# Optimization experiments

Measured on AMD Instinct MI355X. Metric: run time of the kernel, lower is better.

The kernel has to match this reference:

```python
import jax, jax.numpy as jnp
import numpy as np

N, E, F, H, C, G = 50000, 800000, 128, 64, 10, 512
NEG_SLOPE = 0.2
BN_EPS = 1e-5


def setup_inputs() -> dict:
    key = jax.random.key(0)
    ks = jax.random.split(key, 20)
    s = 0.05
    inp = {
        "x": jax.random.normal(ks[0], (N, F), jnp.float32),
        "edge_index": jax.random.randint(ks[1], (2, E), 0, N),
        "batch": jnp.sort(jax.random.randint(ks[2], (N,), 0, G)),
        # GATv2 layer 1 (lin_l, lin_r, att, bias)
        "Wl1": jax.random.normal(ks[3], (H, F), jnp.float32) * s,
        "Wr1": jax.random.normal(ks[4], (H, F), jnp.float32) * s,
        "att1": jax.random.normal(ks[5], (H,), jnp.float32) * s,
        "b1": jnp.zeros((H,), jnp.float32),
        # GATv2 layer 2
        "Wl2": jax.random.normal(ks[6], (H, H), jnp.float32) * s,
        "Wr2": jax.random.normal(ks[7], (H, H), jnp.float32) * s,
        "att2": jax.random.normal(ks[8], (H,), jnp.float32) * s,
        "b2": jnp.zeros((H,), jnp.float32),
        # MLP head: Linear(H,H) -> BatchNorm1d(H) -> ReLU -> Linear(H,C)
        "W3": jax.random.normal(ks[9], (H, H), jnp.float32) * s,
        "b3": jnp.zeros((H,), jnp.float32),
        "gamma": jnp.ones((H,), jnp.float32),
        "beta": jnp.zeros((H,), jnp.float32),
        "W4": jax.random.normal(ks[10], (C, H), jnp.float32) * s,
        "b4": jnp.zeros((C,), jnp.float32),
    }
    return inp


def _gatv2_layer(x, src, dst, Wl, Wr, att, b, n_nodes):
    # GATv2: e_ij = att . LeakyReLU(Wl x_j + Wr x_i); softmax over j in N(i); out_i = sum alpha_ij * Wl x_j
    xl = x @ Wl.T  # [N, H] source transform
    xr = x @ Wr.T  # [N, H] dest transform
    e = jnp.einsum("eh,h->e", jax.nn.leaky_relu(xl[src] + xr[dst], NEG_SLOPE), att)  # [E]
    m = jax.ops.segment_max(e, dst, num_segments=n_nodes)
    m = jnp.where(jnp.isfinite(m), m, 0.0)
    a = jnp.exp(e - m[dst])
    denom = jax.ops.segment_sum(a, dst, num_segments=n_nodes)
    alpha = a / denom[dst]  # self-loops guarantee denom > 0
    out = jax.ops.segment_sum(alpha[:, None] * xl[src], dst, num_segments=n_nodes)
    return out + b


def reference(x, edge_index, batch, Wl1, Wr1, att1, b1, Wl2, Wr2, att2, b2,
              W3, b3, gamma, beta, W4, b4):
    n_nodes = x.shape[0]
    loop = jnp.arange(n_nodes, dtype=edge_index.dtype)
    src = jnp.concatenate([edge_index[0], loop])  # add_self_loops=True (PyG default)
    dst = jnp.concatenate([edge_index[1], loop])

    h = _gatv2_layer(x, src, dst, Wl1, Wr1, att1, b1, n_nodes)
    h = jax.nn.relu(h)
    h = _gatv2_layer(h, src, dst, Wl2, Wr2, att2, b2, n_nodes)

    # global_mean_pool over graphs
    sums = jax.ops.segment_sum(h, batch, num_segments=G)  # [G, H]
    counts = jax.ops.segment_sum(jnp.ones((n_nodes,), h.dtype), batch, num_segments=G)
    pooled = sums / jnp.maximum(counts, 1.0)[:, None]

    # MLP head: Linear -> BatchNorm1d (training: batch stats, biased var) -> ReLU -> Linear
    z = pooled @ W3.T + b3
    mu = jnp.mean(z, axis=0)
    var = jnp.mean((z - mu) ** 2, axis=0)
    z = (z - mu) / jnp.sqrt(var + BN_EPS) * gamma + beta
    z = jax.nn.relu(z)
    z = z @ W4.T + b4
    return jax.nn.log_softmax(z, axis=1)
```

## Files before the change

kernel.cpp:

```cpp
#include <hip/hip_runtime.h>
#include <hip/hip_bf16.h>

#define NODES 50000
#define EDGES 800000
#define FEAT 128
#define HID 64
#define NCLS 10
#define NGRAPH 512
#define ETOT (EDGES + NODES)
#define NEG_SLOPE 0.2f
#define BN_EPS 1e-5f
#define NT_TILES ((NODES + 63) / 64)
#define NBINS 98
#define BTILE 8192
#define BBLK ((ETOT + BTILE - 1) / BTILE)
#define BIN_CAP 14336
#define TBLK 512
#define EDGE_WAVES 8192

typedef __attribute__((ext_vector_type(8))) short short8;
typedef __attribute__((ext_vector_type(4))) float f32x4;

__device__ __forceinline__ short f2b(float v) {
  unsigned int u = __float_as_uint(v);
  return (short)((u + 0x7FFFu + ((u >> 16) & 1u)) >> 16);
}
__device__ __forceinline__ float b2f(short s) {
  return __uint_as_float(((unsigned int)(unsigned short)s) << 16);
}


__device__ __forceinline__ void transform_body(
    char* smem, int bid, const void* __restrict__ A, int a_bf16, int K,
    const float* __restrict__ Wl, const float* __restrict__ Wr,
    short* __restrict__ xl, short* __restrict__ xr) {
  short* s_a = (short*)smem;
  char* dyn2 = smem + 64 * (K + 8) * 2;
  short* s_w = (short*)dyn2;
  float* s_out = (float*)dyn2;
  const int pitch = K + 8;
  int tid = threadIdx.x;
  int w = tid >> 6, lane = tid & 63;
  int n16 = lane & 15, quad = lane >> 4;
  int half = w & 1, chunk = w >> 1;
  short* outp = half ? xr : xl;
  float* s_ow = s_out + w * 16 * 68;
  int ktn = K >> 5;
  int kq = K >> 2, ksh = (K == 128) ? 5 : 4;

  for (int i = tid; i < 128 * kq; i += 512) {
    int r = i / kq, c = i - r * kq;
    const float* src = (r < 64) ? Wl : Wr;
    float4 v = *((const float4*)(src + (r & 63) * K) + c);
    short4 bb;
    bb.x = f2b(v.x); bb.y = f2b(v.y); bb.z = f2b(v.z); bb.w = f2b(v.w);
    *(short4*)(s_w + r * pitch + c * 4) = bb;
  }
  __syncthreads();
  short8 bfrag[4][4];
  for (int t = 0; t < 4; ++t)
    for (int kt = 0; kt < ktn; ++kt)
      bfrag[t][kt] = *(const short8*)(s_w + (half * 64 + t * 16 + n16) * pitch + kt * 32 + quad * 8);

  for (int nt = bid; nt < NT_TILES; nt += TBLK) {
    int n0 = nt * 64;
    __syncthreads();
    if (a_bf16) {
      int ku = K >> 3;
      for (int i = tid; i < 64 * ku; i += 512) {
        int row = i / ku, c = i - row * ku;
        int grow = n0 + row;
        short8 v = (short8){0, 0, 0, 0, 0, 0, 0, 0};
        if (grow < NODES) v = ((const short8*)((const short*)A + (size_t)grow * K))[c];
        *(short8*)(s_a + row * pitch + c * 8) = v;
      }
    } else {
      for (int i = tid; i < (64 << ksh); i += 512) {
        int row = i >> ksh, kc = i & (kq - 1);
        int grow = n0 + row;
        float4 v = (grow < NODES) ? *((const float4*)((const float*)A + (size_t)grow * K) + kc)
                                  : make_float4(0.f, 0.f, 0.f, 0.f);
        short4 bb;
        bb.x = f2b(v.x); bb.y = f2b(v.y); bb.z = f2b(v.z); bb.w = f2b(v.w);
        *(short4*)(s_a + row * pitch + kc * 4) = bb;
      }
    }
    __syncthreads();
    f32x4 acc[4];
#pragma unroll
    for (int t = 0; t < 4; ++t) acc[t] = (f32x4){0.f, 0.f, 0.f, 0.f};
    const short* arow = s_a + (chunk * 16 + n16) * pitch + quad * 8;
    for (int kt = 0; kt < ktn; ++kt) {
      short8 af = *(const short8*)(arow + kt * 32);
#pragma unroll
      for (int t = 0; t < 4; ++t)
        acc[t] = __builtin_amdgcn_mfma_f32_16x16x32_bf16(af, bfrag[t][kt], acc[t], 0, 0, 0);
    }
#pragma unroll
    for (int t = 0; t < 4; ++t)
#pragma unroll
      for (int r = 0; r < 4; ++r)
        s_ow[(quad * 4 + r) * 68 + t * 16 + n16] = acc[t][r];
#pragma unroll
    for (int it = 0; it < 4; ++it) {
      int i = it * 64 + lane;
      int row = i >> 4, c4 = i & 15;
      int grow = n0 + chunk * 16 + row;
      if (grow < NODES) {
        float4 v = *(const float4*)(s_ow + row * 68 + c4 * 4);
        short4 bb;
        bb.x = f2b(v.x); bb.y = f2b(v.y); bb.z = f2b(v.z); bb.w = f2b(v.w);
        *(short4*)(outp + (size_t)grow * HID + c4 * 4) = bb;
      }
    }
  }
}


__device__ __forceinline__ void binscatter_body(
    char* smem, int bid, const int* __restrict__ ei,
    int* __restrict__ binCursor, unsigned int* __restrict__ binned) {
  int* h = (int*)smem;
  int* b0 = h + NBINS;
  int tid = threadIdx.x;
  for (int i = tid; i < NBINS; i += 512) h[i] = 0;
  __syncthreads();
  int base = bid * BTILE;
  for (int k = 0; k < BTILE; k += 512) {
    int i = base + k + tid;
    if (i < ETOT) {
      int d = (i < EDGES) ? ei[EDGES + i] : (i - EDGES);
      atomicAdd(&h[d >> 9], 1);
    }
  }
  __syncthreads();
  for (int i = tid; i < NBINS; i += 512) {
    b0[i] = h[i] ? atomicAdd(&binCursor[i], h[i]) : 0;
    h[i] = 0;
  }
  __syncthreads();
  for (int k = 0; k < BTILE; k += 512) {
    int i = base + k + tid;
    if (i < ETOT) {
      int s, d;
      if (i < EDGES) { s = ei[i]; d = ei[EDGES + i]; }
      else { s = d = i - EDGES; }
      int bin = d >> 9;
      int r = atomicAdd(&h[bin], 1);
      binned[(size_t)bin * BIN_CAP + b0[bin] + r] =
          (unsigned int)s | ((unsigned int)(d & 511) << 16);
    }
  }
}


__global__ void __launch_bounds__(512) k_front(
    const float* __restrict__ x, const float* __restrict__ Wl1,
    const float* __restrict__ Wr1, short* __restrict__ xl, short* __restrict__ xr,
    const int* __restrict__ ei, int* __restrict__ binCursor,
    unsigned int* __restrict__ binned) {
  extern __shared__ char smem[];
  if (blockIdx.x < TBLK)
    transform_body(smem, blockIdx.x, x, 0, FEAT, Wl1, Wr1, xl, xr);
  else
    binscatter_body(smem, blockIdx.x - TBLK, ei, binCursor, binned);
}

__global__ void __launch_bounds__(512) k_transform2(
    const short* __restrict__ h, const float* __restrict__ Wl2,
    const float* __restrict__ Wr2, short* __restrict__ xl, short* __restrict__ xr) {
  extern __shared__ char smem[];
  transform_body(smem, blockIdx.x, h, 1, HID, Wl2, Wr2, xl, xr);
}


__global__ void __launch_bounds__(512) k_csr(
    const int* __restrict__ binCursor, const unsigned int* __restrict__ binned,
    int* __restrict__ rowstart, unsigned short* __restrict__ rowcnt,
    unsigned short* __restrict__ srcs, const int* __restrict__ batch,
    int* __restrict__ gstart) {
  __shared__ int h[512], sc[512], cur[512];
  __shared__ unsigned short sl[BIN_CAP];
  int b = blockIdx.x, t = threadIdx.x;
  if (b == NBINS) {
    for (int g = t; g <= NGRAPH; g += 512) {
      int lo = 0, hi = NODES;
      while (lo < hi) { int mid = (lo + hi) >> 1; if (batch[mid] < g) lo = mid + 1; else hi = mid; }
      gstart[g] = lo;
    }
    return;
  }
  size_t e0 = (size_t)b * BIN_CAP;
  int cnt = binCursor[b];
  int n0 = b << 9;
  h[t] = 0;
  __syncthreads();
  for (int i = t; i < cnt; i += 512)
    atomicAdd(&h[binned[e0 + i] >> 16], 1);
  __syncthreads();
  sc[t] = h[t];
  __syncthreads();
  for (int off = 1; off < 512; off <<= 1) {
    int v = (t >= off) ? sc[t - off] : 0;
    __syncthreads();
    sc[t] += v;
    __syncthreads();
  }
  int excl = sc[t] - h[t];
  cur[t] = excl;
  int node = n0 + t;
  if (node < NODES) {
    rowstart[node] = (int)e0 + excl;
    rowcnt[node] = (unsigned short)h[t];
  }
  __syncthreads();
  for (int i = t; i < cnt; i += 512) {
    unsigned int p = binned[e0 + i];
    int slot = atomicAdd(&cur[p >> 16], 1);
    sl[slot] = (unsigned short)(p & 0xFFFFu);
  }
  __syncthreads();
  for (int i = t; i < cnt; i += 512)
    srcs[e0 + i] = sl[i];
}


__global__ void __launch_bounds__(256) k_edge(
    const int* __restrict__ rowstart, const unsigned short* __restrict__ rowcnt,
    const unsigned short* __restrict__ srcs,
    const short* __restrict__ xlb, const short* __restrict__ xrb,
    const float* __restrict__ att, const float* __restrict__ bias,
    short* __restrict__ outb, int do_relu) {
  int wv = blockIdx.x * 4 + (threadIdx.x >> 6);
  int lane = threadIdx.x & 63;
  int fg = lane & 7;
  int eslot = lane >> 3;
  float at8[8], bb8[8];
  {
    float4 a0 = *(const float4*)(att + fg * 8);
    float4 a1 = *(const float4*)(att + fg * 8 + 4);
    at8[0] = a0.x; at8[1] = a0.y; at8[2] = a0.z; at8[3] = a0.w;
    at8[4] = a1.x; at8[5] = a1.y; at8[6] = a1.z; at8[7] = a1.w;
    float4 b0 = *(const float4*)(bias + fg * 8);
    float4 b1 = *(const float4*)(bias + fg * 8 + 4);
    bb8[0] = b0.x; bb8[1] = b0.y; bb8[2] = b0.z; bb8[3] = b0.w;
    bb8[4] = b1.x; bb8[5] = b1.y; bb8[6] = b1.z; bb8[7] = b1.w;
  }
  int wid = wv;
  if (wid >= NODES) return;
  int nbeg = rowstart[wid];
  int ncnt = rowcnt[wid];
  short8 nxr = *(const short8*)(xrb + (size_t)wid * HID + fg * 8);
  while (true) {
    int beg = nbeg, end = nbeg + ncnt;
    short8 xrs = nxr;
    int nwid = wid + EDGE_WAVES;
    if (nwid < NODES) {
      nbeg = rowstart[nwid];
      ncnt = rowcnt[nwid];
      nxr = *(const short8*)(xrb + (size_t)nwid * HID + fg * 8);
    }
    float xr8[8], acc8[8];
#pragma unroll
    for (int q = 0; q < 8; ++q) { xr8[q] = b2f(xrs[q]); acc8[q] = 0.f; }
    float denom = 0.f;
    for (int base = beg; base < end; base += 64) {
      int cnt = end - base; if (cnt > 64) cnt = 64;
      int myidx = (lane < cnt) ? (int)srcs[base + lane] : 0;
      int j0 = eslot;
      int sP = __shfl(myidx, (j0 < cnt) ? j0 : 0, 64);
      short8 xs = *(const short8*)(xlb + (size_t)sP * HID + fg * 8);
      for (int j = 0; j < cnt; j += 8) {
        bool valid = (j + eslot) < cnt;
        short8 cur = xs;
        if (j + 8 < cnt) {
          int jn = j + 8 + eslot;
          int sn = __shfl(myidx, (jn < cnt) ? jn : 0, 64);
          xs = *(const short8*)(xlb + (size_t)sn * HID + fg * 8);
        }
        float c8[8];
        float part = 0.f;
#pragma unroll
        for (int q = 0; q < 8; ++q) {
          c8[q] = b2f(cur[q]);
          float v = c8[q] + xr8[q];
          v = (v > 0.f) ? v : NEG_SLOPE * v;
          part += v * at8[q];
        }
        part += __shfl_xor(part, 1, 64);
        part += __shfl_xor(part, 2, 64);
        part += __shfl_xor(part, 4, 64);
        float p = valid ? __expf(part) : 0.f;
        denom += p;
#pragma unroll
        for (int q = 0; q < 8; ++q) acc8[q] += p * c8[q];
      }
    }
    denom += __shfl_xor(denom, 8, 64);
    denom += __shfl_xor(denom, 16, 64);
    denom += __shfl_xor(denom, 32, 64);
#pragma unroll
    for (int q = 0; q < 8; ++q) {
      acc8[q] += __shfl_xor(acc8[q], 8, 64);
      acc8[q] += __shfl_xor(acc8[q], 16, 64);
      acc8[q] += __shfl_xor(acc8[q], 32, 64);
    }
    if (eslot == 0) {
      float inv = 1.f / denom;
      short8 o;
#pragma unroll
      for (int q = 0; q < 8; ++q) {
        float ov = acc8[q] * inv + bb8[q];
        if (do_relu) ov = fmaxf(ov, 0.f);
        o[q] = f2b(ov);
      }
      *(short8*)(outb + (size_t)wid * HID + fg * 8) = o;
    }
    if (nwid >= NODES) break;
    wid = nwid;
  }
}


__global__ void k_pool(const short* __restrict__ h, const int* __restrict__ gstart,
                       float* __restrict__ pool) {
  int g = blockIdx.x * (blockDim.x >> 6) + (threadIdx.x >> 6);
  if (g >= NGRAPH) return;
  int lane = threadIdx.x & 63;
  int fg = lane & 7, ns = lane >> 3;
  int beg = gstart[g], end = gstart[g + 1];
  float acc[8] = {0.f, 0.f, 0.f, 0.f, 0.f, 0.f, 0.f, 0.f};
  for (int n = beg + ns; n < end; n += 8) {
    short8 v = *(const short8*)(h + (size_t)n * HID + fg * 8);
#pragma unroll
    for (int q = 0; q < 8; ++q) acc[q] += b2f(v[q]);
  }
#pragma unroll
  for (int q = 0; q < 8; ++q) {
    acc[q] += __shfl_xor(acc[q], 8, 64);
    acc[q] += __shfl_xor(acc[q], 16, 64);
    acc[q] += __shfl_xor(acc[q], 32, 64);
  }
  if (ns == 0) {
    float inv = 1.f / fmaxf((float)(end - beg), 1.f);
    float4 o0 = {acc[0] * inv, acc[1] * inv, acc[2] * inv, acc[3] * inv};
    float4 o1 = {acc[4] * inv, acc[5] * inv, acc[6] * inv, acc[7] * inv};
    *(float4*)(pool + g * HID + fg * 8) = o0;
    *(float4*)(pool + g * HID + fg * 8 + 4) = o1;
  }
}


__global__ void k_head1(const float* __restrict__ pool,
                        const float* __restrict__ W3, const float* __restrict__ b3,
                        float* __restrict__ z) {
  __shared__ float s_w3[HID * (HID + 1)];
  for (int idx = threadIdx.x; idx < HID * HID; idx += blockDim.x) {
    int f = idx >> 6, k = idx & 63;
    s_w3[f * (HID + 1) + k] = W3[idx];
  }
  __syncthreads();
  int i = blockIdx.x * blockDim.x + threadIdx.x;
  if (i >= NGRAPH * HID) return;
  int g = i >> 6, f = i & 63;
  float acc = b3[f];
  for (int k = 0; k < HID; ++k)
    acc += pool[g * HID + k] * s_w3[f * (HID + 1) + k];
  z[i] = acc;
}

__global__ void k_head2(const float* __restrict__ z, const float* __restrict__ gamma,
                        const float* __restrict__ beta, float* __restrict__ ss) {
  int f = threadIdx.x;
  if (f >= HID) return;
  float s = 0.f, s2 = 0.f;
  for (int g = 0; g < NGRAPH; ++g) {
    float v = z[g * HID + f];
    s += v; s2 += v * v;
  }
  float mu = s / NGRAPH;
  float var = s2 / NGRAPH - mu * mu;
  float rstd = rsqrtf(var + BN_EPS);
  float sc = gamma[f] * rstd;
  ss[f] = sc;
  ss[HID + f] = beta[f] - mu * sc;
}

__global__ void k_head3(const float* __restrict__ z, const float* __restrict__ ss,
                        const float* __restrict__ W4, const float* __restrict__ b4,
                        float* __restrict__ out) {
  int g = blockIdx.x * blockDim.x + threadIdx.x;
  if (g >= NGRAPH) return;
  float acc[NCLS];
#pragma unroll
  for (int c = 0; c < NCLS; ++c) acc[c] = b4[c];
  for (int f = 0; f < HID; ++f) {
    float zn = fmaxf(z[g * HID + f] * ss[f] + ss[HID + f], 0.f);
#pragma unroll
    for (int c = 0; c < NCLS; ++c) acc[c] += zn * W4[c * HID + f];
  }
  float m = acc[0];
#pragma unroll
  for (int c = 1; c < NCLS; ++c) m = fmaxf(m, acc[c]);
  float sum = 0.f;
#pragma unroll
  for (int c = 0; c < NCLS; ++c) sum += __expf(acc[c] - m);
  float lse = m + __logf(sum);
#pragma unroll
  for (int c = 0; c < NCLS; ++c) out[g * NCLS + c] = acc[c] - lse;
}

extern "C" void kernel_launch(void* const* d_in, const int* in_sizes, int n_in,
                              void* d_out, int out_size, void* d_ws, size_t ws_size,
                              hipStream_t stream) {
  (void)in_sizes; (void)n_in; (void)out_size; (void)ws_size;
  const float* x     = (const float*)d_in[0];
  const int*   ei    = (const int*)d_in[1];
  const int*   batch = (const int*)d_in[2];
  const float* Wl1   = (const float*)d_in[3];
  const float* Wr1   = (const float*)d_in[4];
  const float* att1  = (const float*)d_in[5];
  const float* b1    = (const float*)d_in[6];
  const float* Wl2   = (const float*)d_in[7];
  const float* Wr2   = (const float*)d_in[8];
  const float* att2  = (const float*)d_in[9];
  const float* b2    = (const float*)d_in[10];
  const float* W3    = (const float*)d_in[11];
  const float* b3    = (const float*)d_in[12];
  const float* gamma = (const float*)d_in[13];
  const float* beta  = (const float*)d_in[14];
  const float* W4    = (const float*)d_in[15];
  const float* b4    = (const float*)d_in[16];
  float* out = (float*)d_out;

  char* ws = (char*)d_ws;
  size_t off = 0;
  auto alloc = [&](size_t bytes) -> char* {
    char* p = ws + off;
    off += (bytes + 255) & ~(size_t)255;
    return p;
  };
  int*      binCursor = (int*)alloc((size_t)NBINS * 4);
  unsigned int*   binned = (unsigned int*)alloc((size_t)NBINS * BIN_CAP * 4);
  unsigned short* srcs   = (unsigned short*)alloc((size_t)NBINS * BIN_CAP * 2);
  int*      rowstart  = (int*)alloc((size_t)NODES * 4);
  unsigned short* rowcnt = (unsigned short*)alloc((size_t)NODES * 2);
  int*      gstart    = (int*)alloc((size_t)(NGRAPH + 1) * 4);
  short*    bufA      = (short*)alloc((size_t)NODES * HID * 2);
  short*    bufB      = (short*)alloc((size_t)NODES * HID * 2);
  short*    bufC      = (short*)alloc((size_t)NODES * HID * 2);
  float*    pool      = (float*)alloc((size_t)NGRAPH * HID * 4);
  float*    z         = (float*)alloc((size_t)NGRAPH * HID * 4);
  float*    ss        = (float*)alloc((size_t)2 * HID * 4);

  int lds1 = 64 * (FEAT + 8) * 2 + 34816;
  int lds2 = 64 * (HID + 8) * 2 + 34816;

  hipMemsetAsync(binCursor, 0, (size_t)NBINS * 4, stream);
  k_front<<<TBLK + BBLK, 512, lds1, stream>>>(x, Wl1, Wr1, bufA, bufB, ei, binCursor, binned);
  k_csr<<<NBINS + 1, 512, 0, stream>>>(binCursor, binned, rowstart, rowcnt, srcs, batch, gstart);
  k_edge<<<EDGE_WAVES / 4, 256, 0, stream>>>(rowstart, rowcnt, srcs, bufA, bufB, att1, b1, bufC, 1);
  k_transform2<<<TBLK, 512, lds2, stream>>>(bufC, Wl2, Wr2, bufA, bufB);
  k_edge<<<EDGE_WAVES / 4, 256, 0, stream>>>(rowstart, rowcnt, srcs, bufA, bufB, att2, b2, bufC, 0);
  k_pool<<<NGRAPH / 4, 256, 0, stream>>>(bufC, gstart, pool);
  k_head1<<<(NGRAPH * HID + 255) / 256, 256, 0, stream>>>(pool, W3, b3, z);
  k_head2<<<1, 64, 0, stream>>>(z, gamma, beta, ss);
  k_head3<<<(NGRAPH + 255) / 256, 256, 0, stream>>>(z, ss, W4, b4, out);
}
```

Baseline: 252.3 us.

## Fuse CSR build into front kernel via spin barrier; merge MLP head kernels

Folds the CSR-building blocks and the graph-start search into the front kernel. The CSR blocks spin on a global done counter until every bin-scatter block has finished, which removes one kernel launch and its boundary. The three head kernels are also merged into a single 512-thread block that keeps W4 and the BN scale/shift in shared memory. The cost is forward-progress risk: the spinning CSR blocks rely on the scatter blocks being scheduled first. The head's 32K-element matmul also becomes serial on one CU.

```diff
diff --git a/kernel.cpp b/kernel.cpp
--- a/kernel.cpp
+++ b/kernel.cpp
@@ -154,42 +154,21 @@
 }
 
 
-__global__ void __launch_bounds__(512) k_front(
-    const float* __restrict__ x, const float* __restrict__ Wl1,
-    const float* __restrict__ Wr1, short* __restrict__ xl, short* __restrict__ xr,
-    const int* __restrict__ ei, int* __restrict__ binCursor,
-    unsigned int* __restrict__ binned) {
-  extern __shared__ char smem[];
-  if (blockIdx.x < TBLK)
-    transform_body(smem, blockIdx.x, x, 0, FEAT, Wl1, Wr1, xl, xr);
-  else
-    binscatter_body(smem, blockIdx.x - TBLK, ei, binCursor, binned);
-}
-
-__global__ void __launch_bounds__(512) k_transform2(
-    const short* __restrict__ h, const float* __restrict__ Wl2,
-    const float* __restrict__ Wr2, short* __restrict__ xl, short* __restrict__ xr) {
-  extern __shared__ char smem[];
-  transform_body(smem, blockIdx.x, h, 1, HID, Wl2, Wr2, xl, xr);
-}
-
-
-__global__ void __launch_bounds__(512) k_csr(
+__device__ __forceinline__ void csr_body(
+    char* smem, int b, int* __restrict__ done,
     const int* __restrict__ binCursor, const unsigned int* __restrict__ binned,
     int* __restrict__ rowstart, unsigned short* __restrict__ rowcnt,
-    unsigned short* __restrict__ srcs, const int* __restrict__ batch,
-    int* __restrict__ gstart) {
-  __shared__ int h[512], sc[512], cur[512];
-  __shared__ unsigned short sl[BIN_CAP];
-  int b = blockIdx.x, t = threadIdx.x;
-  if (b == NBINS) {
-    for (int g = t; g <= NGRAPH; g += 512) {
-      int lo = 0, hi = NODES;
-      while (lo < hi) { int mid = (lo + hi) >> 1; if (batch[mid] < g) lo = mid + 1; else hi = mid; }
-      gstart[g] = lo;
-    }
-    return;
-  }
+    unsigned short* __restrict__ srcs) {
+  int* h = (int*)smem;
+  int* sc = h + 512;
+  int* cur = sc + 512;
+  unsigned short* sl = (unsigned short*)(cur + 512);
+  int t = threadIdx.x;
+  if (t == 0) {
+    while (atomicAdd(done, 0) < BBLK) {}
+  }
+  __syncthreads();
+  __threadfence();
   size_t e0 = (size_t)b * BIN_CAP;
   int cnt = binCursor[b];
   int n0 = b << 9;
@@ -222,6 +201,41 @@
   __syncthreads();
   for (int i = t; i < cnt; i += 512)
     srcs[e0 + i] = sl[i];
+}
+
+
+__global__ void __launch_bounds__(512) k_front(
+    const float* __restrict__ x, const float* __restrict__ Wl1,
+    const float* __restrict__ Wr1, short* __restrict__ xl, short* __restrict__ xr,
+    const int* __restrict__ ei, int* __restrict__ binCursor, int* __restrict__ done,
+    unsigned int* __restrict__ binned, int* __restrict__ rowstart,
+    unsigned short* __restrict__ rowcnt, unsigned short* __restrict__ srcs,
+    const int* __restrict__ batch, int* __restrict__ gstart) {
+  extern __shared__ char smem[];
+  int b = blockIdx.x;
+  if (b < TBLK) {
+    transform_body(smem, b, x, 0, FEAT, Wl1, Wr1, xl, xr);
+  } else if (b < TBLK + BBLK) {
+    binscatter_body(smem, b - TBLK, ei, binCursor, binned);
+    __syncthreads();
+    __threadfence();
+    if (threadIdx.x == 0) atomicAdd(done, 1);
+  } else if (b < TBLK + BBLK + NBINS) {
+    csr_body(smem, b - TBLK - BBLK, done, binCursor, binned, rowstart, rowcnt, srcs);
+  } else {
+    for (int g = threadIdx.x; g <= NGRAPH; g += 512) {
+      int lo = 0, hi = NODES;
+      while (lo < hi) { int mid = (lo + hi) >> 1; if (batch[mid] < g) lo = mid + 1; else hi = mid; }
+      gstart[g] = lo;
+    }
+  }
+}
+
+__global__ void __launch_bounds__(512) k_transform2(
+    const short* __restrict__ h, const float* __restrict__ Wl2,
+    const float* __restrict__ Wr2, short* __restrict__ xl, short* __restrict__ xr) {
+  extern __shared__ char smem[];
+  transform_body(smem, blockIdx.x, h, 1, HID, Wl2, Wr2, xl, xr);
 }
 
 
@@ -351,63 +365,64 @@
 }
 
 
-__global__ void k_head1(const float* __restrict__ pool,
-                        const float* __restrict__ W3, const float* __restrict__ b3,
-                        float* __restrict__ z) {
+__global__ void __launch_bounds__(512) k_headf(
+    const float* __restrict__ pool, const float* __restrict__ W3,
+    const float* __restrict__ b3, const float* __restrict__ gamma,
+    const float* __restrict__ beta, const float* __restrict__ W4,
+    const float* __restrict__ b4, float* __restrict__ z,
+    float* __restrict__ out) {
   __shared__ float s_w3[HID * (HID + 1)];
-  for (int idx = threadIdx.x; idx < HID * HID; idx += blockDim.x) {
+  __shared__ float s_w4[NCLS * HID];
+  __shared__ float s_ss[2 * HID];
+  int t = threadIdx.x;
+  for (int idx = t; idx < HID * HID; idx += 512) {
     int f = idx >> 6, k = idx & 63;
     s_w3[f * (HID + 1) + k] = W3[idx];
   }
-  __syncthreads();
-  int i = blockIdx.x * blockDim.x + threadIdx.x;
-  if (i >= NGRAPH * HID) return;
-  int g = i >> 6, f = i & 63;
-  float acc = b3[f];
-  for (int k = 0; k < HID; ++k)
-    acc += pool[g * HID + k] * s_w3[f * (HID + 1) + k];
-  z[i] = acc;
-}
-
-__global__ void k_head2(const float* __restrict__ z, const float* __restrict__ gamma,
-                        const float* __restrict__ beta, float* __restrict__ ss) {
-  int f = threadIdx.x;
-  if (f >= HID) return;
-  float s = 0.f, s2 = 0.f;
-  for (int g = 0; g < NGRAPH; ++g) {
-    float v = z[g * HID + f];
-    s += v; s2 += v * v;
-  }
-  float mu = s / NGRAPH;
-  float var = s2 / NGRAPH - mu * mu;
-  float rstd = rsqrtf(var + BN_EPS);
-  float sc = gamma[f] * rstd;
-  ss[f] = sc;
-  ss[HID + f] = beta[f] - mu * sc;
-}
-
-__global__ void k_head3(const float* __restrict__ z, const float* __restrict__ ss,
-                        const float* __restrict__ W4, const float* __restrict__ b4,
-                        float* __restrict__ out) {
-  int g = blockIdx.x * blockDim.x + threadIdx.x;
-  if (g >= NGRAPH) return;
-  float acc[NCLS];
-#pragma unroll
-  for (int c = 0; c < NCLS; ++c) acc[c] = b4[c];
-  for (int f = 0; f < HID; ++f) {
-    float zn = fmaxf(z[g * HID + f] * ss[f] + ss[HID + f], 0.f);
-#pragma unroll
-    for (int c = 0; c < NCLS; ++c) acc[c] += zn * W4[c * HID + f];
-  }
-  float m = acc[0];
-#pragma unroll
-  for (int c = 1; c < NCLS; ++c) m = fmaxf(m, acc[c]);
-  float sum = 0.f;
-#pragma unroll
-  for (int c = 0; c < NCLS; ++c) sum += __expf(acc[c] - m);
-  float lse = m + __logf(sum);
-#pragma unroll
-  for (int c = 0; c < NCLS; ++c) out[g * NCLS + c] = acc[c] - lse;
+  for (int idx = t; idx < NCLS * HID; idx += 512) s_w4[idx] = W4[idx];
+  __syncthreads();
+  for (int i = t; i < NGRAPH * HID; i += 512) {
+    int g = i >> 6, f = i & 63;
+    float acc = b3[f];
+    for (int k = 0; k < HID; ++k)
+      acc += pool[g * HID + k] * s_w3[f * (HID + 1) + k];
+    z[i] = acc;
+  }
+  __threadfence_block();
+  __syncthreads();
+  if (t < HID) {
+    float s = 0.f, s2 = 0.f;
+    for (int g = 0; g < NGRAPH; ++g) {
+      float v = z[g * HID + t];
+      s += v; s2 += v * v;
+    }
+    float mu = s / NGRAPH;
+    float var = s2 / NGRAPH - mu * mu;
+    float rstd = rsqrtf(var + BN_EPS);
+    float sc = gamma[t] * rstd;
+    s_ss[t] = sc;
+    s_ss[HID + t] = beta[t] - mu * sc;
+  }
+  __syncthreads();
+  if (t < NGRAPH) {
+    float acc[NCLS];
+#pragma unroll
+    for (int c = 0; c < NCLS; ++c) acc[c] = b4[c];
+    for (int f = 0; f < HID; ++f) {
+      float zn = fmaxf(z[t * HID + f] * s_ss[f] + s_ss[HID + f], 0.f);
+#pragma unroll
+      for (int c = 0; c < NCLS; ++c) acc[c] += zn * s_w4[c * HID + f];
+    }
+    float m = acc[0];
+#pragma unroll
+    for (int c = 1; c < NCLS; ++c) m = fmaxf(m, acc[c]);
+    float sum = 0.f;
+#pragma unroll
+    for (int c = 0; c < NCLS; ++c) sum += __expf(acc[c] - m);
+    float lse = m + __logf(sum);
+#pragma unroll
+    for (int c = 0; c < NCLS; ++c) out[t * NCLS + c] = acc[c] - lse;
+  }
 }
 
 extern "C" void kernel_launch(void* const* d_in, const int* in_sizes, int n_in,
@@ -440,7 +455,8 @@
     off += (bytes + 255) & ~(size_t)255;
     return p;
   };
-  int*      binCursor = (int*)alloc((size_t)NBINS * 4);
+  int*      binCursor = (int*)alloc((size_t)(NBINS + 1) * 4);
+  int*      done      = binCursor + NBINS;
   unsigned int*   binned = (unsigned int*)alloc((size_t)NBINS * BIN_CAP * 4);
   unsigned short* srcs   = (unsigned short*)alloc((size_t)NBINS * BIN_CAP * 2);
   int*      rowstart  = (int*)alloc((size_t)NODES * 4);
@@ -451,19 +467,17 @@
   short*    bufC      = (short*)alloc((size_t)NODES * HID * 2);
   float*    pool      = (float*)alloc((size_t)NGRAPH * HID * 4);
   float*    z         = (float*)alloc((size_t)NGRAPH * HID * 4);
-  float*    ss        = (float*)alloc((size_t)2 * HID * 4);
 
   int lds1 = 64 * (FEAT + 8) * 2 + 34816;
   int lds2 = 64 * (HID + 8) * 2 + 34816;
 
-  hipMemsetAsync(binCursor, 0, (size_t)NBINS * 4, stream);
-  k_front<<<TBLK + BBLK, 512, lds1, stream>>>(x, Wl1, Wr1, bufA, bufB, ei, binCursor, binned);
-  k_csr<<<NBINS + 1, 512, 0, stream>>>(binCursor, binned, rowstart, rowcnt, srcs, batch, gstart);
+  hipMemsetAsync(binCursor, 0, (size_t)(NBINS + 1) * 4, stream);
+  k_front<<<TBLK + BBLK + NBINS + 1, 512, lds1, stream>>>(
+      x, Wl1, Wr1, bufA, bufB, ei, binCursor, done, binned,
+      rowstart, rowcnt, srcs, batch, gstart);
   k_edge<<<EDGE_WAVES / 4, 256, 0, stream>>>(rowstart, rowcnt, srcs, bufA, bufB, att1, b1, bufC, 1);
   k_transform2<<<TBLK, 512, lds2, stream>>>(bufC, Wl2, Wr2, bufA, bufB);
   k_edge<<<EDGE_WAVES / 4, 256, 0, stream>>>(rowstart, rowcnt, srcs, bufA, bufB, att2, b2, bufC, 0);
   k_pool<<<NGRAPH / 4, 256, 0, stream>>>(bufC, gstart, pool);
-  k_head1<<<(NGRAPH * HID + 255) / 256, 256, 0, stream>>>(pool, W3, b3, z);
-  k_head2<<<1, 64, 0, stream>>>(z, gamma, beta, ss);
-  k_head3<<<(NGRAPH + 255) / 256, 256, 0, stream>>>(z, ss, W4, b4, out);
-}
+  k_headf<<<1, 512, 0, stream>>>(pool, W3, b3, gamma, beta, W4, b4, z, out);
+}
```

New measurement: 340.1 us. +34.8%, slower.
